# Optimization experiments

Hardware: AMD Instinct MI355X
Metric: run time of the kernel (lower is better)

Reference implementation:

```python
import jax, jax.numpy as jnp
import numpy as np

N = 4096
IN_DIM = 256
HID = 64
NHEADS = 4
OUT_DIM = 128
ALPHA = 0.5  # LeakyReLU negative slope
NEG_INF = -9e15


def gat_layer(x, mask, W, a, concat):
    """Dense GraphAttentionLayer (pyGAT style).
    x:[N,Fin], mask:[N,N] bool, W:[Fin,Fout], a:[2*Fout]."""
    Wh = x @ W                                   # [N, Fout]
    Fout = W.shape[1]
    f1 = Wh @ a[:Fout]                           # [N]
    f2 = Wh @ a[Fout:]                           # [N]
    e = jax.nn.leaky_relu(f1[:, None] + f2[None, :], negative_slope=ALPHA)  # [N,N]
    att = jax.nn.softmax(jnp.where(mask, e, NEG_INF), axis=1)               # [N,N]
    h = att @ Wh                                 # [N, Fout]
    return jax.nn.elu(h) if concat else h


def setup_inputs() -> dict:
    key = jax.random.key(0)
    ks = jax.random.split(key, 6)
    x = jax.random.normal(ks[0], (N, IN_DIM), dtype=jnp.float32)
    adj = jax.random.randint(ks[1], (N, N), 0, 2, dtype=jnp.int32)
    s_in = 1.0 / np.sqrt(IN_DIM)
    s_hid = 1.0 / np.sqrt(HID * NHEADS)
    W_heads = jax.random.uniform(ks[2], (NHEADS, IN_DIM, HID), jnp.float32, -s_in, s_in)
    a_heads = jax.random.uniform(ks[3], (NHEADS, 2 * HID), jnp.float32, -s_in, s_in)
    W_out = jax.random.uniform(ks[4], (HID * NHEADS, OUT_DIM), jnp.float32, -s_hid, s_hid)
    a_out = jax.random.uniform(ks[5], (2 * OUT_DIM,), jnp.float32, -s_hid, s_hid)
    return {"x": x, "adj": adj, "W_heads": W_heads, "a_heads": a_heads,
            "W_out": W_out, "a_out": a_out}


def reference(x, adj, W_heads, a_heads, W_out, a_out):
    mask = adj > 0
    # multi-head attention, concat along feature dim
    heads = jax.vmap(lambda W, a: gat_layer(x, mask, W, a, True))(W_heads, a_heads)
    h = jnp.transpose(heads, (1, 0, 2)).reshape(N, NHEADS * HID)  # [N, H*HID]
    # dropout=0 -> identity; final GAT layer (concat=False) + outer ELU
    out = jax.nn.elu(gat_layer(h, mask, W_out, a_out, False))     # [N, OUT_DIM]
    return out
```

## Files before the change

kernel.cpp:

```cpp
#include <hip/hip_runtime.h>
#include <hip/hip_bf16.h>

#define N 4096
#define IN_DIM 256
#define HID 64
#define NHEADS 4
#define OUT_DIM 128
#define LOG2E 1.44269504088896340736f

typedef __attribute__((ext_vector_type(8))) short bf16x8;
typedef __attribute__((ext_vector_type(4))) float f32x4;

__global__ void gemm1_kernel(const float* __restrict__ x,
                             const float* __restrict__ W,
                             const float* __restrict__ a,
                             __hip_bfloat16* __restrict__ WhB,
                             float* __restrict__ f1, float* __restrict__ f2) {
    __shared__ float xs[8 * IN_DIM];
    const int t = threadIdx.x;
    const int c = t & 63, h = t >> 6;
    const int i0 = blockIdx.x * 8;
    const float4* xg = (const float4*)(x + (size_t)i0 * IN_DIM);
    float4* xs4 = (float4*)xs;
    for (int u = t; u < 8 * IN_DIM / 4; u += 256) xs4[u] = xg[u];
    __syncthreads();
    float acc[8];
#pragma unroll
    for (int r = 0; r < 8; r++) acc[r] = 0.f;
    const float* Wp = W + (size_t)h * IN_DIM * HID + c;
    for (int k = 0; k < IN_DIM; k += 4) {
        const float w0 = Wp[(size_t)(k + 0) * HID];
        const float w1 = Wp[(size_t)(k + 1) * HID];
        const float w2 = Wp[(size_t)(k + 2) * HID];
        const float w3 = Wp[(size_t)(k + 3) * HID];
#pragma unroll
        for (int r = 0; r < 8; r++) {
            const float4 xv = *(const float4*)(xs + r * IN_DIM + k);
            acc[r] += xv.x * w0 + xv.y * w1 + xv.z * w2 + xv.w * w3;
        }
    }
    union { ushort u[8]; uint4 v; } cv;
#pragma unroll
    for (int r = 0; r < 8; r++)
        cv.u[r] = __hip_bfloat16_raw(__float2bfloat16(acc[r])).x;
    const int jblk = i0 >> 5, quad = (i0 >> 3) & 3;
    const int lane_idx = (c & 15) + 16 * quad;
    *(uint4*)(WhB + ((((size_t)h * (N / 32) + jblk) * 4 + (c >> 4)) * 64 +
                     lane_idx) * 8) = cv.v;
    const float av1 = a[h * 2 * HID + c];
    const float av2 = a[h * 2 * HID + HID + c];
    float s1[8], s2[8];
#pragma unroll
    for (int r = 0; r < 8; r++) { s1[r] = acc[r] * av1; s2[r] = acc[r] * av2; }
#pragma unroll
    for (int mm = 32; mm > 0; mm >>= 1) {
#pragma unroll
        for (int r = 0; r < 8; r++) {
            s1[r] += __shfl_xor(s1[r], mm, 64);
            s2[r] += __shfl_xor(s2[r], mm, 64);
        }
    }
    if (c == 0) {
#pragma unroll
        for (int r = 0; r < 8; r++) {
            f1[(size_t)h * N + i0 + r] = s1[r] * LOG2E;
            f2[(size_t)h * N + i0 + r] = s2[r] * LOG2E;
        }
    }
}

__global__ void mask_kernel(const int* __restrict__ adj,
                            unsigned* __restrict__ maskT) {
    const int lane = threadIdx.x & 63, w = threadIdx.x >> 6;
    const int j0 = blockIdx.x * 64;
    const int i0 = blockIdx.y * 16 + w * 4;
    const int jw0 = j0 >> 5;
#pragma unroll
    for (int rr = 0; rr < 4; rr++) {
        const int i = i0 + rr;
        const int av = adj[(size_t)i * N + j0 + lane];
        const unsigned long long b = __ballot(av > 0);
        if (lane == 0) {
            maskT[(size_t)jw0 * N + i] = (unsigned)b;
            maskT[(size_t)(jw0 + 1) * N + i] = (unsigned)(b >> 32);
        }
    }
}

template <int HEADS, int D, int G, int WPE>
__global__ __launch_bounds__(G * 64, WPE) void attn_fused(
        const unsigned* __restrict__ maskT,
        const __hip_bfloat16* __restrict__ WhB,
        const float* __restrict__ f1g, const float* __restrict__ f2g,
        float* __restrict__ outp) {
    constexpr int CT = D / 16;
    constexpr int CC = (D == 64) ? 1 : 2;
    constexpr int KSTEPS = N / (32 * G);
    __shared__ float sh[G * 16 * CC * 17];
    __shared__ float dsh[G * 16];
    const int t = threadIdx.x;
    const int g = t >> 6, lane = t & 63;
    const int m = lane & 15, quad = lane >> 4;
    const int h = blockIdx.y;
    const int i0 = blockIdx.x * 16;
    const int i = i0 + m;

    const float f1v = f1g[(size_t)h * N + i];
    const float* f2p = f2g + (size_t)h * N;
    const bf16x8* whb = (const bf16x8*)WhB + (size_t)h * (N / 32) * CT * 64;

    const f32x4 zero = {0.f, 0.f, 0.f, 0.f};
    f32x4 acc[CT];
    f32x4 sac = zero;
#pragma unroll
    for (int ct = 0; ct < CT; ct++) acc[ct] = zero;
    const short one_bf = (short)0x3F80;
    const bf16x8 ones = {one_bf, one_bf, one_bf, one_bf,
                         one_bf, one_bf, one_bf, one_bf};

    for (int ks = 0; ks < KSTEPS; ks++) {
        const int j0 = g * (N / G) + ks * 32;
        const int jw = j0 >> 5;
        const unsigned mwrd = maskT[(size_t)jw * N + i];
        const float4 f2lo = *(const float4*)(f2p + j0 + quad * 8);
        const float4 f2hi = *(const float4*)(f2p + j0 + quad * 8 + 4);
        bf16x8 bfrag[CT];
        const bf16x8* bp = whb + (size_t)jw * CT * 64 + lane;
#pragma unroll
        for (int ct = 0; ct < CT; ct++) bfrag[ct] = bp[ct * 64];
        const float f2v[8] = {f2lo.x, f2lo.y, f2lo.z, f2lo.w,
                              f2hi.x, f2hi.y, f2hi.z, f2hi.w};
        float p[8];
#pragma unroll
        for (int e = 0; e < 8; e++) {
            const float tt = f1v + f2v[e];
            const float lr = fmaxf(tt, 0.5f * tt);
            const float pe = __builtin_amdgcn_exp2f(lr);
            p[e] = ((mwrd >> (quad * 8 + e)) & 1u) ? pe : 0.f;
        }
        union { bf16x8 v; __hip_bfloat162 h2[4]; } u;
#pragma unroll
        for (int e2 = 0; e2 < 4; e2++)
            u.h2[e2] = __float22bfloat162_rn(
                make_float2(p[2 * e2], p[2 * e2 + 1]));
        const bf16x8 afr = u.v;
#pragma unroll
        for (int ct = 0; ct < CT; ct++)
            acc[ct] = __builtin_amdgcn_mfma_f32_16x16x32_bf16(
                afr, bfrag[ct], acc[ct], 0, 0, 0);
        sac = __builtin_amdgcn_mfma_f32_16x16x32_bf16(afr, ones, sac, 0, 0, 0);
    }

#pragma unroll
    for (int rd = 0; rd < CT / CC; rd++) {
#pragma unroll
        for (int cc = 0; cc < CC; cc++) {
            const int ct = rd * CC + cc;
#pragma unroll
            for (int r = 0; r < 4; r++)
                sh[((g * 16 + quad * 4 + r) * CC + cc) * 17 + m] = acc[ct][r];
        }
        if (rd == 0 && m == 0) {
#pragma unroll
            for (int r = 0; r < 4; r++) dsh[g * 16 + quad * 4 + r] = sac[r];
        }
        __syncthreads();
        if (t < 256 * CC) {
            int row, ch;
            if (D == 64) { row = t & 15; ch = t >> 4; }
            else         { ch = t & 31; row = (t >> 5) & 15; }
            float av = 0.f, ss = 0.f;
#pragma unroll
            for (int gg = 0; gg < G; gg++) {
                av += sh[((gg * 16 + row) * CC + (ch >> 4)) * 17 + (ch & 15)];
                ss += dsh[gg * 16 + row];
            }
            float v = av / ss;
            v = (v > 0.f) ? v : (__builtin_amdgcn_exp2f(v * LOG2E) - 1.f);
            const int chg = h * D + rd * CC * 16 + ch;
            if (D == 64)
                outp[(size_t)chg * N + i0 + row] = v;
            else
                outp[(size_t)(i0 + row) * D + chg] = v;
        }
        __syncthreads();
    }
}

__global__ void gemm2_kernel(const float* __restrict__ h1T,
                             const float* __restrict__ W2,
                             const float* __restrict__ a2,
                             __hip_bfloat16* __restrict__ WhB2,
                             float* __restrict__ f1, float* __restrict__ f2) {
    __shared__ float hs[8 * IN_DIM];
    __shared__ float fred[2][2][4][2];
    const int t = threadIdx.x;
    const int c = t & 127, rh = t >> 7;
    const int i0 = blockIdx.x * 8;
    for (int u = t; u < 8 * IN_DIM; u += 256) {
        const int r = u & 7, k = u >> 3;
        hs[r * IN_DIM + k] = h1T[(size_t)k * N + i0 + r];
    }
    __syncthreads();
    float acc[4];
#pragma unroll
    for (int rr = 0; rr < 4; rr++) acc[rr] = 0.f;
    for (int k = 0; k < IN_DIM; k += 4) {
        const float w0 = W2[(size_t)(k + 0) * OUT_DIM + c];
        const float w1 = W2[(size_t)(k + 1) * OUT_DIM + c];
        const float w2 = W2[(size_t)(k + 2) * OUT_DIM + c];
        const float w3 = W2[(size_t)(k + 3) * OUT_DIM + c];
#pragma unroll
        for (int rr = 0; rr < 4; rr++) {
            const float4 hv = *(const float4*)(hs + (rh * 4 + rr) * IN_DIM + k);
            acc[rr] += hv.x * w0 + hv.y * w1 + hv.z * w2 + hv.w * w3;
        }
    }
    union { ushort u[4]; uint2 v; } cv;
#pragma unroll
    for (int rr = 0; rr < 4; rr++)
        cv.u[rr] = __hip_bfloat16_raw(__float2bfloat16(acc[rr])).x;
    const int jblk = i0 >> 5, quad = (i0 >> 3) & 3;
    const int lane_idx = (c & 15) + 16 * quad;
    *(uint2*)((__hip_bfloat16*)WhB2 +
              (((size_t)jblk * 8 + (c >> 4)) * 64 + lane_idx) * 8 + rh * 4) = cv.v;
    const float av1 = a2[c], av2 = a2[OUT_DIM + c];
    float s1[4], s2[4];
#pragma unroll
    for (int rr = 0; rr < 4; rr++) { s1[rr] = acc[rr] * av1; s2[rr] = acc[rr] * av2; }
#pragma unroll
    for (int mm = 32; mm > 0; mm >>= 1) {
#pragma unroll
        for (int rr = 0; rr < 4; rr++) {
            s1[rr] += __shfl_xor(s1[rr], mm, 64);
            s2[rr] += __shfl_xor(s2[rr], mm, 64);
        }
    }
    if ((t & 63) == 0) {
        const int chalf = (t >> 6) & 1;
#pragma unroll
        for (int rr = 0; rr < 4; rr++) {
            fred[rh][chalf][rr][0] = s1[rr];
            fred[rh][chalf][rr][1] = s2[rr];
        }
    }
    __syncthreads();
    if (t < 16) {
        const int fn = t & 1, rr = (t >> 1) & 3, rh2 = t >> 3;
        const float v = (fred[rh2][0][rr][fn] + fred[rh2][1][rr][fn]) * LOG2E;
        (fn ? f2 : f1)[i0 + rh2 * 4 + rr] = v;
    }
}

extern "C" void kernel_launch(void* const* d_in, const int* in_sizes, int n_in,
                              void* d_out, int out_size, void* d_ws, size_t ws_size,
                              hipStream_t stream) {
    const float* x   = (const float*)d_in[0];
    const int*   adj = (const int*)d_in[1];
    const float* Wh_ = (const float*)d_in[2];
    const float* ah  = (const float*)d_in[3];
    const float* W2  = (const float*)d_in[4];
    const float* a2  = (const float*)d_in[5];
    float* out = (float*)d_out;

    float* ws = (float*)d_ws;
    float* f1a = ws;
    float* f2a = f1a + (size_t)NHEADS * N;
    float* f1b = f2a + (size_t)NHEADS * N;
    float* f2b = f1b + N;
    float* h1T = f2b + N;
    __hip_bfloat16* WhB1 = (__hip_bfloat16*)(h1T + (size_t)IN_DIM * N);
    __hip_bfloat16* WhB2 = WhB1 + (size_t)NHEADS * HID * N;
    unsigned* maskT = (unsigned*)(WhB2 + (size_t)OUT_DIM * N);

    mask_kernel<<<dim3(N / 64, N / 16), 256, 0, stream>>>(adj, maskT);
    gemm1_kernel<<<N / 8, 256, 0, stream>>>(x, Wh_, ah, WhB1, f1a, f2a);
    attn_fused<NHEADS, HID, 8, 6>
        <<<dim3(N / 16, NHEADS), 512, 0, stream>>>(maskT, WhB1, f1a, f2a, h1T);
    gemm2_kernel<<<N / 8, 256, 0, stream>>>(h1T, W2, a2, WhB2, f1b, f2b);
    attn_fused<1, OUT_DIM, 16, 4>
        <<<dim3(N / 16, 1), 1024, 0, stream>>>(maskT, WhB2, f1b, f2b, out);
}
```

Before: 200.5 us.

## Merge mask and gemm1 into one prep kernel; tile two row groups per attention wave

The mask-packing kernel and the first GEMM become one launch, with blocks split by index. The mask path now reads int4 per lane and bit-interleaves the ballots so a row's mask is built in a single pass. The first attention layer processes two 16-row tiles per wave (MW=2), so each loaded WhB fragment and f2 value is reused across two MFMA row blocks, with fewer waves per block. In exchange, the mask bit order changes and relies on the interleave matching the quad*8+e indexing, and register pressure goes up.

```diff
diff --git a/kernel.cpp b/kernel.cpp
--- a/kernel.cpp
+++ b/kernel.cpp
@@ -11,83 +11,92 @@
 typedef __attribute__((ext_vector_type(8))) short bf16x8;
 typedef __attribute__((ext_vector_type(4))) float f32x4;
 
-__global__ void gemm1_kernel(const float* __restrict__ x,
-                             const float* __restrict__ W,
-                             const float* __restrict__ a,
-                             __hip_bfloat16* __restrict__ WhB,
-                             float* __restrict__ f1, float* __restrict__ f2) {
+__global__ __launch_bounds__(256, 4) void prep_kernel(
+        const float* __restrict__ x, const float* __restrict__ W,
+        const float* __restrict__ a, const int* __restrict__ adj,
+        __hip_bfloat16* __restrict__ WhB,
+        float* __restrict__ f1, float* __restrict__ f2,
+        unsigned* __restrict__ maskT) {
     __shared__ float xs[8 * IN_DIM];
     const int t = threadIdx.x;
-    const int c = t & 63, h = t >> 6;
-    const int i0 = blockIdx.x * 8;
-    const float4* xg = (const float4*)(x + (size_t)i0 * IN_DIM);
-    float4* xs4 = (float4*)xs;
-    for (int u = t; u < 8 * IN_DIM / 4; u += 256) xs4[u] = xg[u];
-    __syncthreads();
-    float acc[8];
-#pragma unroll
-    for (int r = 0; r < 8; r++) acc[r] = 0.f;
-    const float* Wp = W + (size_t)h * IN_DIM * HID + c;
-    for (int k = 0; k < IN_DIM; k += 4) {
-        const float w0 = Wp[(size_t)(k + 0) * HID];
-        const float w1 = Wp[(size_t)(k + 1) * HID];
-        const float w2 = Wp[(size_t)(k + 2) * HID];
-        const float w3 = Wp[(size_t)(k + 3) * HID];
-#pragma unroll
-        for (int r = 0; r < 8; r++) {
-            const float4 xv = *(const float4*)(xs + r * IN_DIM + k);
-            acc[r] += xv.x * w0 + xv.y * w1 + xv.z * w2 + xv.w * w3;
-        }
-    }
-    union { ushort u[8]; uint4 v; } cv;
-#pragma unroll
-    for (int r = 0; r < 8; r++)
-        cv.u[r] = __hip_bfloat16_raw(__float2bfloat16(acc[r])).x;
-    const int jblk = i0 >> 5, quad = (i0 >> 3) & 3;
-    const int lane_idx = (c & 15) + 16 * quad;
-    *(uint4*)(WhB + ((((size_t)h * (N / 32) + jblk) * 4 + (c >> 4)) * 64 +
-                     lane_idx) * 8) = cv.v;
-    const float av1 = a[h * 2 * HID + c];
-    const float av2 = a[h * 2 * HID + HID + c];
-    float s1[8], s2[8];
-#pragma unroll
-    for (int r = 0; r < 8; r++) { s1[r] = acc[r] * av1; s2[r] = acc[r] * av2; }
-#pragma unroll
-    for (int mm = 32; mm > 0; mm >>= 1) {
-#pragma unroll
-        for (int r = 0; r < 8; r++) {
-            s1[r] += __shfl_xor(s1[r], mm, 64);
-            s2[r] += __shfl_xor(s2[r], mm, 64);
-        }
-    }
-    if (c == 0) {
-#pragma unroll
-        for (int r = 0; r < 8; r++) {
-            f1[(size_t)h * N + i0 + r] = s1[r] * LOG2E;
-            f2[(size_t)h * N + i0 + r] = s2[r] * LOG2E;
+    if (blockIdx.x < 512) {
+        const int c = t & 63, h = t >> 6;
+        const int i0 = blockIdx.x * 8;
+        const float4* xg = (const float4*)(x + (size_t)i0 * IN_DIM);
+        float4* xs4 = (float4*)xs;
+        for (int u = t; u < 8 * IN_DIM / 4; u += 256) xs4[u] = xg[u];
+        __syncthreads();
+        float acc[8];
+#pragma unroll
+        for (int r = 0; r < 8; r++) acc[r] = 0.f;
+        const float* Wp = W + (size_t)h * IN_DIM * HID + c;
+        for (int k = 0; k < IN_DIM; k += 4) {
+            const float w0 = Wp[(size_t)(k + 0) * HID];
+            const float w1 = Wp[(size_t)(k + 1) * HID];
+            const float w2 = Wp[(size_t)(k + 2) * HID];
+            const float w3 = Wp[(size_t)(k + 3) * HID];
+#pragma unroll
+            for (int r = 0; r < 8; r++) {
+                const float4 xv = *(const float4*)(xs + r * IN_DIM + k);
+                acc[r] += xv.x * w0 + xv.y * w1 + xv.z * w2 + xv.w * w3;
+            }
+        }
+        union { ushort u[8]; uint4 v; } cv;
+#pragma unroll
+        for (int r = 0; r < 8; r++)
+            cv.u[r] = __hip_bfloat16_raw(__float2bfloat16(acc[r])).x;
+        const int jblk = i0 >> 5, quad = (i0 >> 3) & 3;
+        const int lane_idx = (c & 15) + 16 * quad;
+        *(uint4*)(WhB + ((((size_t)h * (N / 32) + jblk) * 4 + (c >> 4)) * 64 +
+                         lane_idx) * 8) = cv.v;
+        const float av1 = a[h * 2 * HID + c];
+        const float av2 = a[h * 2 * HID + HID + c];
+        float s1[8], s2[8];
+#pragma unroll
+        for (int r = 0; r < 8; r++) { s1[r] = acc[r] * av1; s2[r] = acc[r] * av2; }
+#pragma unroll
+        for (int mm = 32; mm > 0; mm >>= 1) {
+#pragma unroll
+            for (int r = 0; r < 8; r++) {
+                s1[r] += __shfl_xor(s1[r], mm, 64);
+                s2[r] += __shfl_xor(s2[r], mm, 64);
+            }
+        }
+        if (c == 0) {
+#pragma unroll
+            for (int r = 0; r < 8; r++) {
+                f1[(size_t)h * N + i0 + r] = s1[r] * LOG2E;
+                f2[(size_t)h * N + i0 + r] = s2[r] * LOG2E;
+            }
+        }
+    } else {
+        const int lane = t & 63, w = t >> 6;
+        const int i = (blockIdx.x - 512) * 4 + w;
+        const int4* arow = (const int4*)(adj + (size_t)i * N);
+        for (int jb = 0; jb < N / 256; jb++) {
+            const int4 a4 = arow[jb * 64 + lane];
+            unsigned long long bal[4];
+            bal[0] = __ballot(a4.x > 0);
+            bal[1] = __ballot(a4.y > 0);
+            bal[2] = __ballot(a4.z > 0);
+            bal[3] = __ballot(a4.w > 0);
+            if (lane < 8) {
+                unsigned word = 0;
+#pragma unroll
+                for (int e = 0; e < 4; e++) {
+                    unsigned xv = (unsigned)(bal[e] >> (8 * lane)) & 0xFFu;
+                    xv = (xv | (xv << 12)) & 0x000F000Fu;
+                    xv = (xv | (xv << 6))  & 0x03030303u;
+                    xv = (xv | (xv << 3))  & 0x11111111u;
+                    word |= xv << e;
+                }
+                maskT[(size_t)(jb * 8 + lane) * N + i] = word;
+            }
         }
     }
 }
 
-__global__ void mask_kernel(const int* __restrict__ adj,
-                            unsigned* __restrict__ maskT) {
-    const int lane = threadIdx.x & 63, w = threadIdx.x >> 6;
-    const int j0 = blockIdx.x * 64;
-    const int i0 = blockIdx.y * 16 + w * 4;
-    const int jw0 = j0 >> 5;
-#pragma unroll
-    for (int rr = 0; rr < 4; rr++) {
-        const int i = i0 + rr;
-        const int av = adj[(size_t)i * N + j0 + lane];
-        const unsigned long long b = __ballot(av > 0);
-        if (lane == 0) {
-            maskT[(size_t)jw0 * N + i] = (unsigned)b;
-            maskT[(size_t)(jw0 + 1) * N + i] = (unsigned)(b >> 32);
-        }
-    }
-}
-
-template <int HEADS, int D, int G, int WPE>
+template <int HEADS, int D, int G, int MW, int WPE>
 __global__ __launch_bounds__(G * 64, WPE) void attn_fused(
         const unsigned* __restrict__ maskT,
         const __hip_bfloat16* __restrict__ WhB,
@@ -96,24 +105,30 @@
     constexpr int CT = D / 16;
     constexpr int CC = (D == 64) ? 1 : 2;
     constexpr int KSTEPS = N / (32 * G);
-    __shared__ float sh[G * 16 * CC * 17];
-    __shared__ float dsh[G * 16];
+    __shared__ float sh[MW * G * 16 * CC * 17];
+    __shared__ float dsh[MW * G * 16];
     const int t = threadIdx.x;
     const int g = t >> 6, lane = t & 63;
     const int m = lane & 15, quad = lane >> 4;
     const int h = blockIdx.y;
-    const int i0 = blockIdx.x * 16;
-    const int i = i0 + m;
-
-    const float f1v = f1g[(size_t)h * N + i];
+    const int i0 = blockIdx.x * (16 * MW);
+
+    float f1v[MW];
+#pragma unroll
+    for (int mw = 0; mw < MW; mw++)
+        f1v[mw] = f1g[(size_t)h * N + i0 + mw * 16 + m];
     const float* f2p = f2g + (size_t)h * N;
     const bf16x8* whb = (const bf16x8*)WhB + (size_t)h * (N / 32) * CT * 64;
 
     const f32x4 zero = {0.f, 0.f, 0.f, 0.f};
-    f32x4 acc[CT];
-    f32x4 sac = zero;
-#pragma unroll
-    for (int ct = 0; ct < CT; ct++) acc[ct] = zero;
+    f32x4 acc[MW][CT];
+    f32x4 sac[MW];
+#pragma unroll
+    for (int mw = 0; mw < MW; mw++) {
+        sac[mw] = zero;
+#pragma unroll
+        for (int ct = 0; ct < CT; ct++) acc[mw][ct] = zero;
+    }
     const short one_bf = (short)0x3F80;
     const bf16x8 ones = {one_bf, one_bf, one_bf, one_bf,
                          one_bf, one_bf, one_bf, one_bf};
@@ -121,7 +136,10 @@
     for (int ks = 0; ks < KSTEPS; ks++) {
         const int j0 = g * (N / G) + ks * 32;
         const int jw = j0 >> 5;
-        const unsigned mwrd = maskT[(size_t)jw * N + i];
+        unsigned mwrd[MW];
+#pragma unroll
+        for (int mw = 0; mw < MW; mw++)
+            mwrd[mw] = maskT[(size_t)jw * N + i0 + mw * 16 + m];
         const float4 f2lo = *(const float4*)(f2p + j0 + quad * 8);
         const float4 f2hi = *(const float4*)(f2p + j0 + quad * 8 + 4);
         bf16x8 bfrag[CT];
@@ -130,58 +148,76 @@
         for (int ct = 0; ct < CT; ct++) bfrag[ct] = bp[ct * 64];
         const float f2v[8] = {f2lo.x, f2lo.y, f2lo.z, f2lo.w,
                               f2hi.x, f2hi.y, f2hi.z, f2hi.w};
-        float p[8];
-#pragma unroll
-        for (int e = 0; e < 8; e++) {
-            const float tt = f1v + f2v[e];
-            const float lr = fmaxf(tt, 0.5f * tt);
-            const float pe = __builtin_amdgcn_exp2f(lr);
-            p[e] = ((mwrd >> (quad * 8 + e)) & 1u) ? pe : 0.f;
-        }
-        union { bf16x8 v; __hip_bfloat162 h2[4]; } u;
-#pragma unroll
-        for (int e2 = 0; e2 < 4; e2++)
-            u.h2[e2] = __float22bfloat162_rn(
-                make_float2(p[2 * e2], p[2 * e2 + 1]));
-        const bf16x8 afr = u.v;
+        bf16x8 afr[MW];
+#pragma unroll
+        for (int mw = 0; mw < MW; mw++) {
+            float p[8];
+#pragma unroll
+            for (int e = 0; e < 8; e++) {
+                const float tt = f1v[mw] + f2v[e];
+                const float lr = fmaxf(tt, 0.5f * tt);
+                const float pe = __builtin_amdgcn_exp2f(lr);
+                p[e] = ((mwrd[mw] >> (quad * 8 + e)) & 1u) ? pe : 0.f;
+            }
+            union { bf16x8 v; __hip_bfloat162 h2[4]; } u;
+#pragma unroll
+            for (int e2 = 0; e2 < 4; e2++)
+                u.h2[e2] = __float22bfloat162_rn(
+                    make_float2(p[2 * e2], p[2 * e2 + 1]));
+            afr[mw] = u.v;
+        }
 #pragma unroll
         for (int ct = 0; ct < CT; ct++)
-            acc[ct] = __builtin_amdgcn_mfma_f32_16x16x32_bf16(
-                afr, bfrag[ct], acc[ct], 0, 0, 0);
-        sac = __builtin_amdgcn_mfma_f32_16x16x32_bf16(afr, ones, sac, 0, 0, 0);
+#pragma unroll
+            for (int mw = 0; mw < MW; mw++)
+                acc[mw][ct] = __builtin_amdgcn_mfma_f32_16x16x32_bf16(
+                    afr[mw], bfrag[ct], acc[mw][ct], 0, 0, 0);
+#pragma unroll
+        for (int mw = 0; mw < MW; mw++)
+            sac[mw] = __builtin_amdgcn_mfma_f32_16x16x32_bf16(
+                afr[mw], ones, sac[mw], 0, 0, 0);
     }
 
 #pragma unroll
     for (int rd = 0; rd < CT / CC; rd++) {
 #pragma unroll
-        for (int cc = 0; cc < CC; cc++) {
-            const int ct = rd * CC + cc;
-#pragma unroll
-            for (int r = 0; r < 4; r++)
-                sh[((g * 16 + quad * 4 + r) * CC + cc) * 17 + m] = acc[ct][r];
-        }
-        if (rd == 0 && m == 0) {
-#pragma unroll
-            for (int r = 0; r < 4; r++) dsh[g * 16 + quad * 4 + r] = sac[r];
+        for (int mw = 0; mw < MW; mw++) {
+#pragma unroll
+            for (int cc = 0; cc < CC; cc++) {
+#pragma unroll
+                for (int r = 0; r < 4; r++)
+                    sh[(((mw * G + g) * 16 + quad * 4 + r) * CC + cc) * 17 + m] =
+                        acc[mw][rd * CC + cc][r];
+            }
+            if (rd == 0 && m == 0) {
+#pragma unroll
+                for (int r = 0; r < 4; r++)
+                    dsh[(mw * G + g) * 16 + quad * 4 + r] = sac[mw][r];
+            }
         }
         __syncthreads();
-        if (t < 256 * CC) {
-            int row, ch;
-            if (D == 64) { row = t & 15; ch = t >> 4; }
-            else         { ch = t & 31; row = (t >> 5) & 15; }
-            float av = 0.f, ss = 0.f;
-#pragma unroll
-            for (int gg = 0; gg < G; gg++) {
-                av += sh[((gg * 16 + row) * CC + (ch >> 4)) * 17 + (ch & 15)];
-                ss += dsh[gg * 16 + row];
-            }
-            float v = av / ss;
-            v = (v > 0.f) ? v : (__builtin_amdgcn_exp2f(v * LOG2E) - 1.f);
-            const int chg = h * D + rd * CC * 16 + ch;
-            if (D == 64)
-                outp[(size_t)chg * N + i0 + row] = v;
-            else
-                outp[(size_t)(i0 + row) * D + chg] = v;
+        if (t < 16 * CC * 16) {
+            int row, chl;
+            if (D == 64) { row = t & 15; chl = (t >> 4) & 15; }
+            else         { chl = t & 31; row = (t >> 5) & 15; }
+#pragma unroll
+            for (int mw = 0; mw < MW; mw++) {
+                float av = 0.f, ss = 0.f;
+#pragma unroll
+                for (int gg = 0; gg < G; gg++) {
+                    av += sh[(((mw * G + gg) * 16 + row) * CC + (chl >> 4)) * 17 +
+                             (chl & 15)];
+                    ss += dsh[(mw * G + gg) * 16 + row];
+                }
+                float v = av / ss;
+                v = (v > 0.f) ? v : (__builtin_amdgcn_exp2f(v * LOG2E) - 1.f);
+                const int chg = h * D + rd * CC * 16 + chl;
+                const int irow = i0 + mw * 16 + row;
+                if (D == 64)
+                    outp[(size_t)chg * N + irow] = v;
+                else
+                    outp[(size_t)irow * D + chg] = v;
+            }
         }
         __syncthreads();
     }
@@ -273,11 +309,10 @@
     __hip_bfloat16* WhB2 = WhB1 + (size_t)NHEADS * HID * N;
     unsigned* maskT = (unsigned*)(WhB2 + (size_t)OUT_DIM * N);
 
-    mask_kernel<<<dim3(N / 64, N / 16), 256, 0, stream>>>(adj, maskT);
-    gemm1_kernel<<<N / 8, 256, 0, stream>>>(x, Wh_, ah, WhB1, f1a, f2a);
-    attn_fused<NHEADS, HID, 8, 6>
-        <<<dim3(N / 16, NHEADS), 512, 0, stream>>>(maskT, WhB1, f1a, f2a, h1T);
+    prep_kernel<<<1536, 256, 0, stream>>>(x, Wh_, ah, adj, WhB1, f1a, f2a, maskT);
+    attn_fused<NHEADS, HID, 4, 2, 4>
+        <<<dim3(N / 32, NHEADS), 256, 0, stream>>>(maskT, WhB1, f1a, f2a, h1T);
     gemm2_kernel<<<N / 8, 256, 0, stream>>>(h1T, W2, a2, WhB2, f1b, f2b);
-    attn_fused<1, OUT_DIM, 16, 4>
+    attn_fused<1, OUT_DIM, 16, 1, 4>
         <<<dim3(N / 16, 1), 1024, 0, stream>>>(maskT, WhB2, f1b, f2b, out);
 }
```

Result: faster. 196.2 us (-2.2%).
